# Performance work log

Measured on AMD Instinct MI355X. Metric: run time of the kernel, lower is better.

The kernel has to match this reference:

```python
import jax, jax.numpy as jnp
import numpy as np

LIMIT = 20      # module's self.limit: only first 20 unique labels per mask participate
EPS = 1e-5      # BatchNorm2d default eps


def _ccl(mask):
    """4-connected component labeling via max-label propagation.
    mask: [H, W] bool. Returns int32 labels, 0 = background; each component's
    label is (1 + max flat pixel index) inside it, so jnp.sort order matches
    torch.unique's ascending order up to a component permutation."""
    H, W = mask.shape
    init = jnp.where(mask, jnp.arange(1, H * W + 1, dtype=jnp.int32).reshape(H, W), 0)

    def prop(l):
        up = jnp.pad(l[1:, :], ((0, 1), (0, 0)))
        dn = jnp.pad(l[:-1, :], ((1, 0), (0, 0)))
        lf = jnp.pad(l[:, 1:], ((0, 0), (0, 1)))
        rt = jnp.pad(l[:, :-1], ((0, 0), (1, 0)))
        m = jnp.maximum(jnp.maximum(l, up), jnp.maximum(dn, jnp.maximum(lf, rt)))
        return jnp.where(mask, m, 0)

    def cond(st):
        return ~st[1]

    def body(st):
        l, _ = st
        nl = prop(l)
        return nl, jnp.all(nl == l)

    labels, _ = jax.lax.while_loop(cond, body, (init, jnp.array(False)))
    return labels


def _region_stats(xb, labels):
    """Compact-rank the LIMIT smallest unique labels (rank 0 = background 0)
    and compute per-component means of xb over pixels.
    xb: [C, H, W]; labels: [H, W] int32.
    Returns means [LIMIT, C], has [LIMIT] bool, seg [P] (LIMIT = dump)."""
    P = labels.size
    lab = labels.reshape(P)
    order = jnp.argsort(lab)
    s = lab[order]
    isnew = jnp.concatenate([jnp.ones((1,), bool), s[1:] != s[:-1]])
    rank_sorted = (jnp.cumsum(isnew) - 1).astype(jnp.int32)  # ascending-unique rank
    rank = jnp.zeros((P,), jnp.int32).at[order].set(rank_sorted)
    valid = (rank < LIMIT) & (lab > 0)   # rank 0 is background label 0
    seg = jnp.where(valid, rank, LIMIT)
    C = xb.shape[0]
    xf = xb.reshape(C, P).T              # [P, C]
    sums = jax.ops.segment_sum(xf, seg, num_segments=LIMIT + 1)[:LIMIT]
    cnts = jax.ops.segment_sum(jnp.ones((P,), xb.dtype), seg, num_segments=LIMIT + 1)[:LIMIT]
    means = sums / jnp.maximum(cnts, 1.0)[:, None]
    has = cnts > 0
    return means, has, seg


def _forward(x, conv_w, conv_b, gamma, beta):
    # attn conv (3x3, SAME) + Softmax2d (softmax over channels)
    logits = jax.lax.conv_general_dilated(
        x, conv_w, (1, 1), 'SAME', dimension_numbers=('NCHW', 'OIHW', 'NCHW')
    ) + conv_b[None, :, None, None]
    out_attn = jax.nn.softmax(logits, axis=1)
    am = jnp.argmax(out_attn, axis=1)            # [B, H, W]
    lab1 = jax.vmap(_ccl)(am == 1)
    lab2 = jax.vmap(_ccl)(am == 2)

    def per_batch(xb, l1, l2):
        m1, h1, s1 = _region_stats(xb, l1)       # means indexed by uniq rank (rank0=bg)
        m2, h2, s2 = _region_stats(xb, l2)
        M = m1 @ m2.T                             # M[i, j] = mean_i . mean_j, mm[i-1, j-1] in torch
        pf = jnp.where(h1[:, None] & h2[None, :], 1.0 + M, 1.0)
        # Each valid (i, j) pair multiplies area1(i) and area2(j) by (1 + mm);
        # sequential in-place updates compound into these closed-form products.
        mult1 = jnp.prod(pf, axis=1)              # [LIMIT]
        mult2 = jnp.prod(pf, axis=0)
        f1 = jnp.where(s1 < LIMIT, mult1[jnp.clip(s1, 0, LIMIT - 1)], 1.0)
        f2 = jnp.where(s2 < LIMIT, mult2[jnp.clip(s2, 0, LIMIT - 1)], 1.0)
        return (f1 * f2).reshape(l1.shape)

    factor = jax.vmap(per_batch)(x, lab1, lab2)  # [B, H, W]
    x2 = x * factor[:, None, :, :]
    # BatchNorm2d in training mode (batch stats, biased var)
    mean = x2.mean(axis=(0, 2, 3))
    var = x2.var(axis=(0, 2, 3))
    xn = (x2 - mean[None, :, None, None]) * jax.lax.rsqrt(var + EPS)[None, :, None, None]
    xn = xn * gamma[None, :, None, None] + beta[None, :, None, None]
    return xn, out_attn


def setup_inputs() -> dict:
    key = jax.random.key(0)
    k1, k2 = jax.random.split(key)
    B, C, H, W = 8, 256, 160, 160
    x = jax.random.normal(k1, (B, C, H, W), dtype=jnp.float32)
    conv_w = jax.random.normal(k2, (3, C, 3, 3), dtype=jnp.float32) * 0.05
    conv_b = jnp.zeros((3,), jnp.float32)
    gamma = jnp.ones((C,), jnp.float32)
    beta = jnp.zeros((C,), jnp.float32)
    return {'x': x, 'conv_w': conv_w, 'conv_b': conv_b, 'gamma': gamma, 'beta': beta}


def reference(x, conv_w, conv_b, gamma, beta):
    return _forward(x, conv_w, conv_b, gamma, beta)
```

## Files before the change

### kernel.cpp

```cpp
#include <hip/hip_runtime.h>
#include <stdint.h>
#include <float.h>

#define HW 160
#define PP 25600
#define BB 8
#define CCH 256
#define NIMG 16
#define LIM 20
#define MAXC 12800
#define CPG 32
#define NCG (CCH/CPG)
#define ROWS 8
#define RT (HW/ROWS)

typedef unsigned char u8;
typedef unsigned long long u64;

__global__ void kzero(float* binsA, float* binsB, int* cnts, int* ncomp,
                      double* sumA, double* sumB, int* lcnt){
  int i = blockIdx.x*256 + threadIdx.x;
  if(i < BB*40*CCH){ binsA[i]=0.f; binsB[i]=0.f; }
  if(i < BB*40) cnts[i]=0;
  if(i < NIMG) ncomp[i]=0;
  if(i < CCH){ sumA[i]=0.0; sumB[i]=0.0; }
  if(i < BB) lcnt[i]=0;
}

__global__ __launch_bounds__(256,4) void kconv(const float* __restrict__ x,
                                               const float* __restrict__ w,
                                               float* __restrict__ partial,
                                               double* __restrict__ sumA,
                                               double* __restrict__ sumB){
  const int b = blockIdx.z, cg = blockIdx.y, r0 = blockIdx.x*ROWS;
  const int tid = threadIdx.x;
  __shared__ float wl[CPG][28];
  __shared__ float xt[10][164];
  __shared__ float bsA[CPG], bsB[CPG];
  for(int t=tid; t<CPG*27; t+=256){
    int cc=t/27, k=t%27;
    wl[cc][k] = w[((k/9)*CCH + cg*CPG + cc)*9 + (k%9)];
  }
  for(int i=tid; i<10*164; i+=256) ((float*)xt)[i]=0.f;
  if(tid<CPG){ bsA[tid]=0.f; bsB[tid]=0.f; }

  const int or_ = tid>>5;
  const int j0  = (tid&31)*5;

  const int f0=2*tid, f1=f0+1;
  const int lr0=f0/40, co0=(f0%40)*4, gr0=r0-1+lr0;
  const int lr1=f1/40, co1=(f1%40)*4, gr1=r0-1+lr1;
  const bool st  = (tid<200);
  const bool ok0 = st && gr0>=0 && gr0<HW;
  const bool ok1 = st && gr1>=0 && gr1<HW;
  const bool insum = (tid>=20 && tid<180);

  const float* xg = x + ((size_t)b*CCH + cg*CPG)*PP;
  float4 v0=make_float4(0.f,0.f,0.f,0.f), v1=v0;
  if(ok0) v0 = *(const float4*)(xg + gr0*HW + co0);
  if(ok1) v1 = *(const float4*)(xg + gr1*HW + co1);

  float acc[3][5];
  #pragma unroll
  for(int o=0;o<3;o++){
    #pragma unroll
    for(int px=0;px<5;px++) acc[o][px]=0.f;
  }

  for(int cc=0; cc<CPG; cc++){
    __syncthreads();
    if(ok0) *(float4*)&xt[lr0][co0] = v0;
    if(ok1) *(float4*)&xt[lr1][co1] = v1;
    __syncthreads();
    float4 n0=make_float4(0.f,0.f,0.f,0.f), n1=n0;
    if(cc+1<CPG){
      const float* xc = xg + (size_t)(cc+1)*PP;
      if(ok0) n0 = *(const float4*)(xc + gr0*HW + co0);
      if(ok1) n1 = *(const float4*)(xc + gr1*HW + co1);
    }
    float s=0.f, s2=0.f;
    if(insum){
      s  = v0.x+v0.y+v0.z+v0.w + v1.x+v1.y+v1.z+v1.w;
      s2 = v0.x*v0.x+v0.y*v0.y+v0.z*v0.z+v0.w*v0.w
         + v1.x*v1.x+v1.y*v1.y+v1.z*v1.z+v1.w*v1.w;
    }
    #pragma unroll
    for(int off=32; off; off>>=1){ s += __shfl_xor(s,off); s2 += __shfl_xor(s2,off); }
    if((tid&63)==0){ atomicAdd(&bsA[cc], s); atomicAdd(&bsB[cc], s2); }
    float sv[3][7];
    #pragma unroll
    for(int rr=0;rr<3;rr++){
      sv[rr][0] = (j0>0) ? xt[or_+rr][j0-1] : 0.f;
      #pragma unroll
      for(int k=1;k<7;k++) sv[rr][k] = xt[or_+rr][j0-1+k];
    }
    #pragma unroll
    for(int o=0;o<3;o++){
      #pragma unroll
      for(int rr=0;rr<3;rr++){
        float w0 = wl[cc][o*9+rr*3+0];
        float w1 = wl[cc][o*9+rr*3+1];
        float w2 = wl[cc][o*9+rr*3+2];
        #pragma unroll
        for(int px=0;px<5;px++)
          acc[o][px] = fmaf(w0, sv[rr][px], fmaf(w1, sv[rr][px+1], fmaf(w2, sv[rr][px+2], acc[o][px])));
      }
    }
    v0=n0; v1=n1;
  }
  __syncthreads();
  if(tid<CPG){
    atomicAdd(&sumA[cg*CPG+tid], (double)bsA[tid]);
    atomicAdd(&sumB[cg*CPG+tid], (double)bsB[tid]);
  }
  size_t base = ((size_t)(cg*BB+b)*3)*PP + (size_t)(r0+or_)*HW + j0;
  #pragma unroll
  for(int o=0;o<3;o++){
    #pragma unroll
    for(int px=0;px<5;px++) partial[base + (size_t)o*PP + px] = acc[o][px];
  }
}

__global__ void ksoftmax(const float* __restrict__ partial, const float* __restrict__ cb,
                         float* __restrict__ attn, u8* __restrict__ am,
                         int* __restrict__ parent, int* __restrict__ maxidx){
  int idx = blockIdx.x*256 + threadIdx.x;
  if(idx >= BB*PP) return;
  int b = idx/PP, p = idx%PP;
  float l[3];
  #pragma unroll
  for(int o=0;o<3;o++){
    float s = cb[o];
    #pragma unroll
    for(int cg=0;cg<NCG;cg++) s += partial[(((size_t)cg*BB+b)*3+o)*PP + p];
    l[o]=s;
  }
  int a=0; float best=l[0];
  if(l[1]>best){best=l[1];a=1;}
  if(l[2]>best){best=l[2];a=2;}
  float e0=__expf(l[0]-best);
  float e1=__expf(l[1]-best);
  float e2=__expf(l[2]-best);
  float inv = 1.f/(e0+e1+e2);
  attn[((size_t)b*3+0)*PP+p]=e0*inv;
  attn[((size_t)b*3+1)*PP+p]=e1*inv;
  attn[((size_t)b*3+2)*PP+p]=e2*inv;
  am[idx]=(u8)a;
  int i1 = (b*2+0)*PP + p, i2 = (b*2+1)*PP + p;
  parent[i1] = (a==1) ? p : -1;
  parent[i2] = (a==2) ? p : -1;
  maxidx[i1] = -1;
  maxidx[i2] = -1;
}

__device__ inline int froot(int* par, int x){
  while(true){
    int p = par[x];
    if(p == x) return x;
    int g = par[p];
    if(g == p) return p;
    par[x] = g;
    x = g;
  }
}
__device__ inline void unite(int* par, int a, int b){
  int ra = froot(par,a), rb = froot(par,b);
  while(ra != rb){
    if(ra > rb){ int t=ra; ra=rb; rb=t; }
    int old = atomicCAS(&par[rb], rb, ra);
    if(old == rb) return;
    rb = froot(par, old);
    ra = froot(par, ra);
  }
}
__global__ void kunion(int* parent){
  int idx = blockIdx.x*256 + threadIdx.x;
  if(idx >= NIMG*PP) return;
  int img = idx/PP, p = idx%PP;
  int* par = parent + img*PP;
  if(par[p] < 0) return;
  int i = p/HW, j = p%HW;
  if(j < HW-1 && par[p+1] >= 0) unite(par, p, p+1);
  if(i < HW-1 && par[p+HW] >= 0) unite(par, p, p+HW);
}
__global__ void kflatmax(int* parent, int* __restrict__ maxidx){
  int idx = blockIdx.x*256 + threadIdx.x;
  if(idx >= NIMG*PP) return;
  int img = idx/PP, p = idx%PP;
  int* par = parent + img*PP;
  if(par[p] < 0) return;
  int r = froot(par, p);
  par[p] = r;
  atomicMax(&maxidx[img*PP + r], p);
}

__global__ void kcompact(const int* __restrict__ parent, const int* __restrict__ maxidx,
                         int* __restrict__ rootlist, int* __restrict__ ncomp){
  int idx = blockIdx.x*256 + threadIdx.x;
  int img = idx/PP, p = idx%PP;
  bool isroot = (parent[idx] == p);
  u64 mask = __ballot(isroot);
  int lane = threadIdx.x & 63;
  int wid = threadIdx.x >> 6;
  __shared__ int wcnt[4];
  __shared__ int bbase;
  if(lane == 0) wcnt[wid] = __popcll(mask);
  __syncthreads();
  if(threadIdx.x == 0){
    int tot = wcnt[0]+wcnt[1]+wcnt[2]+wcnt[3];
    bbase = (tot>0) ? atomicAdd(&ncomp[img], tot) : 0;
  }
  __syncthreads();
  if(isroot){
    int mybase = bbase;
    for(int wv=0; wv<wid; wv++) mybase += wcnt[wv];
    mybase += __popcll(mask & ((lane==63)? ~0ull>>1 : ((1ull<<lane)-1)));
    rootlist[img*MAXC + mybase] = (maxidx[idx]<<16) | p;
  }
}

__global__ __launch_bounds__(256) void kselect(const int* __restrict__ rootlist, const int* __restrict__ ncomp,
                        const int* __restrict__ parent,
                        int* __restrict__ selr, int* __restrict__ nsel){
  int img = blockIdx.x, t = threadIdx.x;
  __shared__ int sv[256];
  __shared__ int scnt[256];
  const int* par = parent + img*PP;
  int cnt=0;
  for(int p=t; p<PP; p+=256) cnt += (par[p]>=0) ? 1 : 0;
  scnt[t]=cnt; __syncthreads();
  for(int off=128; off; off>>=1){ if(t<off) scnt[t]+=scnt[t+off]; __syncthreads(); }
  int K = LIM - ((scnt[0] < PP) ? 1 : 0);
  int nr = ncomp[img];
  const int* rl = rootlist + img*MAXC;
  int prev = -1, n = 0;
  for(int k=0;k<K;k++){
    int best = 0x7fffffff;
    for(int q=t; q<nr; q+=256){ int v=rl[q]; if(v>prev && v<best) best=v; }
    sv[t]=best; __syncthreads();
    for(int off=128; off; off>>=1){
      if(t<off && sv[t+off]<sv[t]) sv[t]=sv[t+off];
      __syncthreads();
    }
    int bv = sv[0]; __syncthreads();
    if(bv == 0x7fffffff) break;
    if(t==0) selr[img*LIM+k] = bv & 0xffff;
    prev = bv; n = k+1;
  }
  if(t==0) nsel[img] = n;
}

__global__ void kseg(const u8* __restrict__ am, const int* __restrict__ parent,
                     const int* __restrict__ selr, const int* __restrict__ nsel,
                     u8* __restrict__ seg, int* __restrict__ cnts,
                     int* __restrict__ list, int* __restrict__ lcnt){
  int idx = blockIdx.x*256 + threadIdx.x;
  __shared__ int cl[40];
  if(threadIdx.x < 40) cl[threadIdx.x] = 0;
  __syncthreads();
  int b = idx/PP, p = idx%PP;
  int a = am[idx];
  int code = 40;
  if(a > 0){
    int img = b*2 + a - 1;
    int r = parent[img*PP + p];
    int n = nsel[img];
    for(int k=0;k<n;k++){
      if(selr[img*LIM + k] == r){ code = (a-1)*LIM + k; break; }
    }
  }
  seg[idx] = (u8)code;
  if(code < 40){
    atomicAdd(&cl[code], 1);
    int pos = atomicAdd(&lcnt[b], 1);
    list[b*PP + pos] = (code<<16) | p;
  }
  __syncthreads();
  if(threadIdx.x < 40 && cl[threadIdx.x] > 0) atomicAdd(&cnts[b*40 + threadIdx.x], cl[threadIdx.x]);
}

__global__ __launch_bounds__(256) void kbins2(const float* __restrict__ x, const int* __restrict__ list,
                                              const int* __restrict__ lcnt,
                                              float* __restrict__ binsA, float* __restrict__ binsB){
  const int b = blockIdx.y;
  const int n = lcnt[b];
  const int c = threadIdx.x;
  for(int e = blockIdx.x; e < n; e += gridDim.x){
    int ent = list[b*PP + e];
    int p = ent & 0xffff;
    int code = ent >> 16;
    float v = x[((size_t)b*CCH + c)*PP + p];
    atomicAdd(&binsA[((size_t)b*40 + code)*CCH + c], v);
    atomicAdd(&binsB[((size_t)b*40 + code)*CCH + c], v*v);
  }
}

__global__ __launch_bounds__(256) void kmult(const float* __restrict__ binsA, const int* __restrict__ cnts,
                       const int* __restrict__ nsel, double* __restrict__ multd,
                       float* __restrict__ multf){
  const int b = blockIdx.x, t = threadIdx.x;
  __shared__ float m1[LIM][CCH+1], m2[LIM][CCH+1];
  __shared__ float Ml[LIM*LIM];
  const int n1 = nsel[b*2+0], n2 = nsel[b*2+1];
  for(int k=0;k<LIM;k++){
    m1[k][t] = (k<n1) ? binsA[((size_t)b*40 + k)*CCH + t] / (float)cnts[b*40 + k] : 0.f;
    m2[k][t] = (k<n2) ? binsA[((size_t)b*40 + LIM + k)*CCH + t] / (float)cnts[b*40 + LIM + k] : 0.f;
  }
  __syncthreads();
  for(int pid=t; pid<LIM*LIM; pid+=256){
    int i = pid/LIM, j = pid%LIM;
    float d = 0.f;
    for(int c=0;c<CCH;c++) d += m1[i][c]*m2[j][c];
    Ml[pid] = 1.f + d;
  }
  __syncthreads();
  if(t < LIM){
    double pr=1.0;
    for(int j=0;j<LIM;j++) pr *= (double)Ml[t*LIM+j];
    multd[b*40 + t] = pr;
    multf[b*40 + t] = (float)pr;
  } else if(t>=64 && t<64+LIM){
    int j=t-64; double pr=1.0;
    for(int i=0;i<LIM;i++) pr *= (double)Ml[i*LIM+j];
    multd[b*40 + LIM + j] = pr;
    multf[b*40 + LIM + j] = (float)pr;
  }
}

__global__ void kscale(const float* __restrict__ binsA, const float* __restrict__ binsB,
                       const double* __restrict__ sumA, const double* __restrict__ sumB,
                       const double* __restrict__ multd, const float* __restrict__ gamma,
                       const float* __restrict__ beta, float* __restrict__ scale, float* __restrict__ shift){
  int c = threadIdx.x;
  double s = sumA[c], s2 = sumB[c];
  for(int b=0;b<BB;b++){
    for(int sc=0; sc<40; sc++){
      double f = multd[b*40+sc];
      s  += (f-1.0)   * (double)binsA[((size_t)b*40+sc)*CCH + c];
      s2 += (f*f-1.0) * (double)binsB[((size_t)b*40+sc)*CCH + c];
    }
  }
  const double N = (double)BB*PP;
  double mean = s/N;
  double devsq = s2 - N*mean*mean;
  bool ovf = !(devsq <= 3.3e38) || !(fabs(s) <= 3.3e38) || !(s2 < 1e300);
  if(ovf){
    scale[c] = 0.f;
    shift[c] = beta[c];
  } else {
    double var = devsq/N;
    double inv = 1.0 / sqrt(var + 1e-5);
    float scv = (float)inv * gamma[c];
    scale[c] = scv;
    shift[c] = beta[c] - (float)mean * scv;
  }
}

__global__ __launch_bounds__(256) void kout(const float* __restrict__ x, const u8* __restrict__ seg,
                      const float* __restrict__ multf, const float* __restrict__ scale,
                      const float* __restrict__ shift, float* __restrict__ out){
  size_t idx = ((size_t)blockIdx.x*256 + threadIdx.x)*4;
  int b = (int)(idx / ((size_t)CCH*PP));
  int c = (int)((idx / PP) % CCH);
  int p = (int)(idx % PP);
  __shared__ float fm[41];
  if(threadIdx.x <= 40) fm[threadIdx.x] = (threadIdx.x<40) ? multf[b*40 + threadIdx.x] : 1.f;
  __syncthreads();
  float sc = scale[c], sh = shift[c];
  float4 o;
  if(sc == 0.f){
    o.x = sh; o.y = sh; o.z = sh; o.w = sh;
  } else {
    float4 xv = *(const float4*)(x + idx);
    uchar4 sv = *(const uchar4*)(seg + (size_t)b*PP + p);
    o.x = xv.x * fm[sv.x] * sc + sh;
    o.y = xv.y * fm[sv.y] * sc + sh;
    o.z = xv.z * fm[sv.z] * sc + sh;
    o.w = xv.w * fm[sv.w] * sc + sh;
  }
  *(float4*)(out + idx) = o;
}

extern "C" void kernel_launch(void* const* d_in, const int* in_sizes, int n_in,
                              void* d_out, int out_size, void* d_ws, size_t ws_size,
                              hipStream_t stream){
  (void)in_sizes; (void)n_in; (void)out_size; (void)ws_size;
  const float* x  = (const float*)d_in[0];
  const float* w  = (const float*)d_in[1];
  const float* cb = (const float*)d_in[2];
  const float* gamma = (const float*)d_in[3];
  const float* beta  = (const float*)d_in[4];
  float* out  = (float*)d_out;
  float* attn = out + (size_t)BB*CCH*PP;

  float* partial  = out;
  int*   parent   = (int*)(out + 20000000);
  int*   maxidx   = (int*)(out + 20500000);
  u8*    am       = (u8*)(out + 21000000);
  float* binsA    = out + 21100000;
  float* binsB    = out + 21200000;
  int*   rootlist = (int*)(out + 21300000);
  int*   ncomp    = (int*)(out + 21600000);
  int*   list     = (int*)(out + 21700000);
  int*   lcnt     = (int*)(out + 22000000);
  double* sumA    = (double*)(out + 22100000);
  double* sumB    = (double*)(out + 22101000);

  double* multd = (double*)d_ws;
  float* multf  = (float*)((char*)d_ws + 2560);
  float* scale  = multf + BB*40;
  float* shift  = scale + CCH;
  int* selr     = (int*)(shift + CCH);
  int* nsel     = selr + NIMG*LIM;
  int* cnts     = nsel + NIMG;
  u8* seg       = (u8*)(cnts + BB*40);

  kzero<<<dim3(320), dim3(256), 0, stream>>>(binsA, binsB, cnts, ncomp, sumA, sumB, lcnt);
  kconv<<<dim3(RT,NCG,BB), dim3(256), 0, stream>>>(x, w, partial, sumA, sumB);
  ksoftmax<<<dim3(800), dim3(256), 0, stream>>>(partial, cb, attn, am, parent, maxidx);
  kunion<<<dim3(1600), dim3(256), 0, stream>>>(parent);
  kflatmax<<<dim3(1600), dim3(256), 0, stream>>>(parent, maxidx);
  kcompact<<<dim3(1600), dim3(256), 0, stream>>>(parent, maxidx, rootlist, ncomp);
  kselect<<<dim3(NIMG), dim3(256), 0, stream>>>(rootlist, ncomp, parent, selr, nsel);
  kseg<<<dim3(800), dim3(256), 0, stream>>>(am, parent, selr, nsel, seg, cnts, list, lcnt);
  kbins2<<<dim3(64,BB), dim3(256), 0, stream>>>(x, list, lcnt, binsA, binsB);
  kmult<<<dim3(BB), dim3(256), 0, stream>>>(binsA, cnts, nsel, multd, multf);
  kscale<<<dim3(1), dim3(256), 0, stream>>>(binsA, binsB, sumA, sumB, multd, gamma, beta, scale, shift);
  kout<<<dim3(51200), dim3(256), 0, stream>>>(x, seg, multf, scale, shift, out);
}
```

Before: 309.1 us.

## Retile attention conv: two output rows per thread, double-buffered LDS tile

The conv kernel now gives each thread two output rows (16-row tiles, 16 channels per group) and double-buffers the shared-memory input tile, so there is one barrier per channel instead of two. Loading four input rows per thread for two outputs cuts the redundant halo reads from LDS. Channel sums are now computed from the LDS tile with per-wave slots instead of shared atomics. In exchange NCG doubles, so the partial buffer is larger and the softmax pass has more partials to reduce, and register pressure rises.

```diff
diff --git a/kernel.cpp b/kernel.cpp
--- a/kernel.cpp
+++ b/kernel.cpp
@@ -9,9 +9,9 @@
 #define NIMG 16
 #define LIM 20
 #define MAXC 12800
-#define CPG 32
+#define CPG 16
 #define NCG (CCH/CPG)
-#define ROWS 8
+#define ROWS 16
 #define RT (HW/ROWS)
 
 typedef unsigned char u8;
@@ -35,89 +35,105 @@
   const int b = blockIdx.z, cg = blockIdx.y, r0 = blockIdx.x*ROWS;
   const int tid = threadIdx.x;
   __shared__ float wl[CPG][28];
-  __shared__ float xt[10][164];
-  __shared__ float bsA[CPG], bsB[CPG];
+  __shared__ float xt[2][18][164];
+  __shared__ float bsA[CPG][4], bsB[CPG][4];
   for(int t=tid; t<CPG*27; t+=256){
     int cc=t/27, k=t%27;
     wl[cc][k] = w[((k/9)*CCH + cg*CPG + cc)*9 + (k%9)];
   }
-  for(int i=tid; i<10*164; i+=256) ((float*)xt)[i]=0.f;
-  if(tid<CPG){ bsA[tid]=0.f; bsB[tid]=0.f; }
-
-  const int or_ = tid>>5;
-  const int j0  = (tid&31)*5;
-
-  const int f0=2*tid, f1=f0+1;
+  for(int i=tid; i<2*18*164; i+=256) ((float*)xt)[i]=0.f;
+  if(tid<CPG*4){ ((float*)bsA)[tid]=0.f; ((float*)bsB)[tid]=0.f; }
+
+  const int f0=tid, f1=tid+256, f2=tid+512;
   const int lr0=f0/40, co0=(f0%40)*4, gr0=r0-1+lr0;
   const int lr1=f1/40, co1=(f1%40)*4, gr1=r0-1+lr1;
-  const bool st  = (tid<200);
-  const bool ok0 = st && gr0>=0 && gr0<HW;
-  const bool ok1 = st && gr1>=0 && gr1<HW;
-  const bool insum = (tid>=20 && tid<180);
-
+  const int lr2=f2/40, co2=(f2%40)*4, gr2=r0-1+lr2;
+  const bool ok0 = gr0>=0 && gr0<HW;
+  const bool ok1 = gr1>=0 && gr1<HW;
+  const bool ok2 = (f2<720) && gr2>=0 && gr2<HW;
   const float* xg = x + ((size_t)b*CCH + cg*CPG)*PP;
-  float4 v0=make_float4(0.f,0.f,0.f,0.f), v1=v0;
-  if(ok0) v0 = *(const float4*)(xg + gr0*HW + co0);
-  if(ok1) v1 = *(const float4*)(xg + gr1*HW + co1);
-
-  float acc[3][5];
+
+  const int band = tid>>5, l32 = tid&31, j0 = l32*5, or0 = band*2;
+  const int wid = tid>>6, lane = tid&63;
+
+  float4 v0, v1, v2;
+  #define LD(cc_) { const float* xc_ = xg + (size_t)(cc_)*PP; \
+    v0 = ok0 ? *(const float4*)(xc_ + gr0*HW + co0) : make_float4(0.f,0.f,0.f,0.f); \
+    v1 = ok1 ? *(const float4*)(xc_ + gr1*HW + co1) : make_float4(0.f,0.f,0.f,0.f); \
+    v2 = ok2 ? *(const float4*)(xc_ + gr2*HW + co2) : make_float4(0.f,0.f,0.f,0.f); }
+  #define STW(buf_) { \
+    if(ok0) *(float4*)&xt[buf_][lr0][co0] = v0; \
+    if(ok1) *(float4*)&xt[buf_][lr1][co1] = v1; \
+    if(ok2) *(float4*)&xt[buf_][lr2][co2] = v2; }
+
+  LD(0);
+  __syncthreads();
+  STW(0);
+  __syncthreads();
+
+  float acc[2][3][5];
   #pragma unroll
-  for(int o=0;o<3;o++){
-    #pragma unroll
-    for(int px=0;px<5;px++) acc[o][px]=0.f;
-  }
-
+  for(int r=0;r<2;r++)
+    #pragma unroll
+    for(int o=0;o<3;o++)
+      #pragma unroll
+      for(int px=0;px<5;px++) acc[r][o][px]=0.f;
+
+  int cur=0;
   for(int cc=0; cc<CPG; cc++){
-    __syncthreads();
-    if(ok0) *(float4*)&xt[lr0][co0] = v0;
-    if(ok1) *(float4*)&xt[lr1][co1] = v1;
-    __syncthreads();
-    float4 n0=make_float4(0.f,0.f,0.f,0.f), n1=n0;
-    if(cc+1<CPG){
-      const float* xc = xg + (size_t)(cc+1)*PP;
-      if(ok0) n0 = *(const float4*)(xc + gr0*HW + co0);
-      if(ok1) n1 = *(const float4*)(xc + gr1*HW + co1);
+    if(cc+1<CPG) LD(cc+1);
+    float sv[4][7];
+    #pragma unroll
+    for(int rr=0;rr<4;rr++){
+      sv[rr][0] = (j0>0) ? xt[cur][or0+rr][j0-1] : 0.f;
+      #pragma unroll
+      for(int k=1;k<7;k++) sv[rr][k] = xt[cur][or0+rr][j0-1+k];
     }
     float s=0.f, s2=0.f;
-    if(insum){
-      s  = v0.x+v0.y+v0.z+v0.w + v1.x+v1.y+v1.z+v1.w;
-      s2 = v0.x*v0.x+v0.y*v0.y+v0.z*v0.z+v0.w*v0.w
-         + v1.x*v1.x+v1.y*v1.y+v1.z*v1.z+v1.w*v1.w;
-    }
+    #pragma unroll
+    for(int rr=1;rr<3;rr++)
+      #pragma unroll
+      for(int k=1;k<6;k++){ float vv=sv[rr][k]; s+=vv; s2=fmaf(vv,vv,s2); }
     #pragma unroll
     for(int off=32; off; off>>=1){ s += __shfl_xor(s,off); s2 += __shfl_xor(s2,off); }
-    if((tid&63)==0){ atomicAdd(&bsA[cc], s); atomicAdd(&bsB[cc], s2); }
-    float sv[3][7];
-    #pragma unroll
-    for(int rr=0;rr<3;rr++){
-      sv[rr][0] = (j0>0) ? xt[or_+rr][j0-1] : 0.f;
-      #pragma unroll
-      for(int k=1;k<7;k++) sv[rr][k] = xt[or_+rr][j0-1+k];
-    }
+    if(lane==0){ bsA[cc][wid] += s; bsB[cc][wid] += s2; }
     #pragma unroll
     for(int o=0;o<3;o++){
       #pragma unroll
-      for(int rr=0;rr<3;rr++){
-        float w0 = wl[cc][o*9+rr*3+0];
-        float w1 = wl[cc][o*9+rr*3+1];
-        float w2 = wl[cc][o*9+rr*3+2];
+      for(int kr=0;kr<3;kr++){
+        float w0 = wl[cc][o*9+kr*3+0];
+        float w1 = wl[cc][o*9+kr*3+1];
+        float w2 = wl[cc][o*9+kr*3+2];
         #pragma unroll
-        for(int px=0;px<5;px++)
-          acc[o][px] = fmaf(w0, sv[rr][px], fmaf(w1, sv[rr][px+1], fmaf(w2, sv[rr][px+2], acc[o][px])));
+        for(int ro=0;ro<2;ro++){
+          #pragma unroll
+          for(int px=0;px<5;px++)
+            acc[ro][o][px] = fmaf(w0, sv[ro+kr][px], fmaf(w1, sv[ro+kr][px+1], fmaf(w2, sv[ro+kr][px+2], acc[ro][o][px])));
+        }
       }
     }
-    v0=n0; v1=n1;
-  }
-  __syncthreads();
-  if(tid<CPG){
-    atomicAdd(&sumA[cg*CPG+tid], (double)bsA[tid]);
-    atomicAdd(&sumB[cg*CPG+tid], (double)bsB[tid]);
-  }
-  size_t base = ((size_t)(cg*BB+b)*3)*PP + (size_t)(r0+or_)*HW + j0;
+    if(cc+1<CPG) STW(cur^1);
+    __syncthreads();
+    cur ^= 1;
+  }
+  #undef LD
+  #undef STW
+
+  if(tid < CPG){
+    float a = bsA[tid][0]+bsA[tid][1]+bsA[tid][2]+bsA[tid][3];
+    float bq = bsB[tid][0]+bsB[tid][1]+bsB[tid][2]+bsB[tid][3];
+    atomicAdd(&sumA[cg*CPG+tid], (double)a);
+    atomicAdd(&sumB[cg*CPG+tid], (double)bq);
+  }
+  size_t base = ((size_t)(cg*BB+b)*3)*PP;
   #pragma unroll
-  for(int o=0;o<3;o++){
-    #pragma unroll
-    for(int px=0;px<5;px++) partial[base + (size_t)o*PP + px] = acc[o][px];
+  for(int ro=0;ro<2;ro++){
+    #pragma unroll
+    for(int o=0;o<3;o++){
+      #pragma unroll
+      for(int px=0;px<5;px++)
+        partial[base + (size_t)o*PP + (size_t)(r0+or0+ro)*HW + j0+px] = acc[ro][o][px];
+    }
   }
 }
 
```

Result: slower. 345.5 us (+11.8%).

## Double-buffer conv input tile and compute channel stats from shared tile

Applied to the files above, without the earlier changes.

The 3x3 attention conv kernel now double-buffers the shared input tile with a two-deep register prefetch, so each channel iteration needs one barrier instead of two. The per-channel sum and sum-of-squares are now taken from the interior values each thread already reads from shared memory, and are accumulated into per-wavefront slots rather than through shared atomics. The launch-bounds occupancy hint is dropped and shared memory use roughly doubles, which may reduce occupancy and raise register pressure.

```diff
diff --git a/kernel.cpp b/kernel.cpp
--- a/kernel.cpp
+++ b/kernel.cpp
@@ -27,25 +27,22 @@
   if(i < BB) lcnt[i]=0;
 }
 
-__global__ __launch_bounds__(256,4) void kconv(const float* __restrict__ x,
-                                               const float* __restrict__ w,
-                                               float* __restrict__ partial,
-                                               double* __restrict__ sumA,
-                                               double* __restrict__ sumB){
+__global__ __launch_bounds__(256) void kconv(const float* __restrict__ x,
+                                             const float* __restrict__ w,
+                                             float* __restrict__ partial,
+                                             double* __restrict__ sumA,
+                                             double* __restrict__ sumB){
   const int b = blockIdx.z, cg = blockIdx.y, r0 = blockIdx.x*ROWS;
   const int tid = threadIdx.x;
   __shared__ float wl[CPG][28];
-  __shared__ float xt[10][164];
-  __shared__ float bsA[CPG], bsB[CPG];
+  __shared__ float xt[2][10][164];
+  __shared__ float bsA[CPG][4], bsB[CPG][4];
   for(int t=tid; t<CPG*27; t+=256){
     int cc=t/27, k=t%27;
     wl[cc][k] = w[((k/9)*CCH + cg*CPG + cc)*9 + (k%9)];
   }
-  for(int i=tid; i<10*164; i+=256) ((float*)xt)[i]=0.f;
-  if(tid<CPG){ bsA[tid]=0.f; bsB[tid]=0.f; }
-
-  const int or_ = tid>>5;
-  const int j0  = (tid&31)*5;
+  for(int i=tid; i<2*10*164; i+=256) ((float*)xt)[i]=0.f;
+  if(tid<CPG*4){ ((float*)bsA)[tid]=0.f; ((float*)bsB)[tid]=0.f; }
 
   const int f0=2*tid, f1=f0+1;
   const int lr0=f0/40, co0=(f0%40)*4, gr0=r0-1+lr0;
@@ -53,65 +50,79 @@
   const bool st  = (tid<200);
   const bool ok0 = st && gr0>=0 && gr0<HW;
   const bool ok1 = st && gr1>=0 && gr1<HW;
-  const bool insum = (tid>=20 && tid<180);
-
   const float* xg = x + ((size_t)b*CCH + cg*CPG)*PP;
-  float4 v0=make_float4(0.f,0.f,0.f,0.f), v1=v0;
-  if(ok0) v0 = *(const float4*)(xg + gr0*HW + co0);
-  if(ok1) v1 = *(const float4*)(xg + gr1*HW + co1);
+
+  const int or_ = tid>>5, j0 = (tid&31)*5;
+  const int wid = tid>>6, lane = tid&63;
+
+  float4 p0, p1, q0, q1;
+  #define LDP(cc_) { const float* xc_ = xg + (size_t)(cc_)*PP; \
+    p0 = ok0 ? *(const float4*)(xc_ + gr0*HW + co0) : make_float4(0.f,0.f,0.f,0.f); \
+    p1 = ok1 ? *(const float4*)(xc_ + gr1*HW + co1) : make_float4(0.f,0.f,0.f,0.f); }
+  #define LDQ(cc_) { const float* xc_ = xg + (size_t)(cc_)*PP; \
+    q0 = ok0 ? *(const float4*)(xc_ + gr0*HW + co0) : make_float4(0.f,0.f,0.f,0.f); \
+    q1 = ok1 ? *(const float4*)(xc_ + gr1*HW + co1) : make_float4(0.f,0.f,0.f,0.f); }
+  #define STWP(buf_) { \
+    if(ok0) *(float4*)&xt[buf_][lr0][co0] = p0; \
+    if(ok1) *(float4*)&xt[buf_][lr1][co1] = p1; }
+
+  LDP(0);
+  __syncthreads();
+  STWP(0);
+  LDP(1);
+  __syncthreads();
 
   float acc[3][5];
   #pragma unroll
-  for(int o=0;o<3;o++){
+  for(int o=0;o<3;o++)
     #pragma unroll
     for(int px=0;px<5;px++) acc[o][px]=0.f;
-  }
-
+
+  int cur=0;
   for(int cc=0; cc<CPG; cc++){
-    __syncthreads();
-    if(ok0) *(float4*)&xt[lr0][co0] = v0;
-    if(ok1) *(float4*)&xt[lr1][co1] = v1;
-    __syncthreads();
-    float4 n0=make_float4(0.f,0.f,0.f,0.f), n1=n0;
-    if(cc+1<CPG){
-      const float* xc = xg + (size_t)(cc+1)*PP;
-      if(ok0) n0 = *(const float4*)(xc + gr0*HW + co0);
-      if(ok1) n1 = *(const float4*)(xc + gr1*HW + co1);
+    if(cc+2<CPG) LDQ(cc+2);
+    float sv[3][7];
+    #pragma unroll
+    for(int rr=0;rr<3;rr++){
+      sv[rr][0] = (j0>0) ? xt[cur][or_+rr][j0-1] : 0.f;
+      #pragma unroll
+      for(int k=1;k<7;k++) sv[rr][k] = xt[cur][or_+rr][j0-1+k];
     }
     float s=0.f, s2=0.f;
-    if(insum){
-      s  = v0.x+v0.y+v0.z+v0.w + v1.x+v1.y+v1.z+v1.w;
-      s2 = v0.x*v0.x+v0.y*v0.y+v0.z*v0.z+v0.w*v0.w
-         + v1.x*v1.x+v1.y*v1.y+v1.z*v1.z+v1.w*v1.w;
-    }
+    #pragma unroll
+    for(int k=1;k<6;k++){ float vv=sv[1][k]; s+=vv; s2=fmaf(vv,vv,s2); }
     #pragma unroll
     for(int off=32; off; off>>=1){ s += __shfl_xor(s,off); s2 += __shfl_xor(s2,off); }
-    if((tid&63)==0){ atomicAdd(&bsA[cc], s); atomicAdd(&bsB[cc], s2); }
-    float sv[3][7];
-    #pragma unroll
-    for(int rr=0;rr<3;rr++){
-      sv[rr][0] = (j0>0) ? xt[or_+rr][j0-1] : 0.f;
-      #pragma unroll
-      for(int k=1;k<7;k++) sv[rr][k] = xt[or_+rr][j0-1+k];
-    }
+    if(lane==0){ bsA[cc][wid] += s; bsB[cc][wid] += s2; }
     #pragma unroll
     for(int o=0;o<3;o++){
       #pragma unroll
-      for(int rr=0;rr<3;rr++){
-        float w0 = wl[cc][o*9+rr*3+0];
-        float w1 = wl[cc][o*9+rr*3+1];
-        float w2 = wl[cc][o*9+rr*3+2];
+      for(int kr=0;kr<3;kr++){
+        float w0 = wl[cc][o*9+kr*3+0];
+        float w1 = wl[cc][o*9+kr*3+1];
+        float w2 = wl[cc][o*9+kr*3+2];
         #pragma unroll
         for(int px=0;px<5;px++)
-          acc[o][px] = fmaf(w0, sv[rr][px], fmaf(w1, sv[rr][px+1], fmaf(w2, sv[rr][px+2], acc[o][px])));
+          acc[o][px] = fmaf(w0, sv[kr][px], fmaf(w1, sv[kr][px+1], fmaf(w2, sv[kr][px+2], acc[o][px])));
       }
     }
-    v0=n0; v1=n1;
-  }
-  __syncthreads();
-  if(tid<CPG){
-    atomicAdd(&sumA[cg*CPG+tid], (double)bsA[tid]);
-    atomicAdd(&sumB[cg*CPG+tid], (double)bsB[tid]);
+    if(cc+1<CPG){
+      STWP(cur^1);
+      __syncthreads();
+      p0=q0; p1=q1;
+      cur ^= 1;
+    }
+  }
+  #undef LDP
+  #undef LDQ
+  #undef STWP
+
+  __syncthreads();
+  if(tid < CPG){
+    float a = bsA[tid][0]+bsA[tid][1]+bsA[tid][2]+bsA[tid][3];
+    float bq = bsB[tid][0]+bsB[tid][1]+bsB[tid][2]+bsB[tid][3];
+    atomicAdd(&sumA[cg*CPG+tid], (double)a);
+    atomicAdd(&sumB[cg*CPG+tid], (double)bq);
   }
   size_t base = ((size_t)(cg*BB+b)*3)*PP + (size_t)(r0+or_)*HW + j0;
   #pragma unroll
```

Measured after the change: 279.3 us. 1.11x faster.
